# Kernel optimization log

Measured on AMD Instinct MI355X. Metric: run time of the kernel, lower is better.

Reference implementation:

```python
import jax, jax.numpy as jnp
import numpy as np

EMBED_DIM_LIST = (192, 384, 576, 768)
MAX_EMBED_DIM = 768
VOCAB = 50257
BATCH, SEQ = 8, 2048


def setup_inputs() -> dict:
    key = jax.random.key(0)
    k1, k2, k3 = jax.random.split(key, 3)
    x = jax.random.randint(k1, (BATCH, SEQ), 0, VOCAB, dtype=jnp.int64)
    weights = jax.random.uniform(k2, (len(EMBED_DIM_LIST),), dtype=jnp.float32)
    emb_weight = jax.random.normal(k3, (VOCAB, MAX_EMBED_DIM), dtype=jnp.float32) * 0.02
    return {"x": x, "weights": weights, "emb_weight": emb_weight}


def reference(x, weights, emb_weight):
    # Faithful to the non-argmax branch:
    #   mixture = sum_i pad(weights[i] * W[:, :d_i], to max_embed_dim)
    # Equivalent vectorized form: column j gets scale sum_i weights[i]*[j < d_i].
    dims = jnp.asarray(EMBED_DIM_LIST)                      # [n_choices]
    col = jnp.arange(MAX_EMBED_DIM)                          # [D]
    mask = (col[None, :] < dims[:, None]).astype(weights.dtype)  # [n_choices, D]
    col_scale = weights @ mask                               # [D]
    embedding_mixture = emb_weight * col_scale[None, :]      # [V, D]
    out = embedding_mixture[x]                               # [B, S, D] gather
    return out
```

## Files before the change

### kernel.cpp

```cpp
#include <hip/hip_runtime.h>

typedef float float4v __attribute__((ext_vector_type(4)));

__global__ void mixed_embed_kernel(const int* __restrict__ x,
                                   const float* __restrict__ w,
                                   const float* __restrict__ emb,
                                   float* __restrict__ out,
                                   int n_vec) {
    const int gid = blockIdx.x * blockDim.x + threadIdx.x;
    if (gid >= n_vec) return;

    const float w0 = w[0], w1 = w[1], w2 = w[2], w3 = w[3];

    const int token = gid / 192;
    const int d4    = gid - token * 192;
    const int row   = x[token];

    const float4v v = reinterpret_cast<const float4v*>(emb)[(long)row * 192 + d4];

    float s = w3;
    s += (d4 < 144) ? w2 : 0.0f;
    s += (d4 <  96) ? w1 : 0.0f;
    s += (d4 <  48) ? w0 : 0.0f;

    float4v o = v;
    o[0] *= s; o[1] *= s; o[2] *= s; o[3] *= s;
    __builtin_nontemporal_store(o, reinterpret_cast<float4v*>(out) + gid);
}

extern "C" void kernel_launch(void* const* d_in, const int* in_sizes, int n_in,
                              void* d_out, int out_size, void* d_ws, size_t ws_size,
                              hipStream_t stream) {
    const int*   x   = (const int*)d_in[0];
    const float* w   = (const float*)d_in[1];
    const float* emb = (const float*)d_in[2];
    float*       out = (float*)d_out;

    const int n_vec = out_size / 4;
    const int block = 256;
    const int grid  = (n_vec + block - 1) / block;

    mixed_embed_kernel<<<grid, block, 0, stream>>>(x, w, emb, out, n_vec);
}
```

Measured before the change: 21.04 us.

## Assign one wavefront per token with three float4 loads per lane

```diff
diff --git a/kernel.cpp b/kernel.cpp
--- a/kernel.cpp
+++ b/kernel.cpp
@@ -2,30 +2,40 @@
 
 typedef float float4v __attribute__((ext_vector_type(4)));
 
-__global__ void mixed_embed_kernel(const int* __restrict__ x,
-                                   const float* __restrict__ w,
-                                   const float* __restrict__ emb,
-                                   float* __restrict__ out,
-                                   int n_vec) {
-    const int gid = blockIdx.x * blockDim.x + threadIdx.x;
-    if (gid >= n_vec) return;
+__global__ void __launch_bounds__(256) mixed_embed_kernel(
+    const int* __restrict__ x,
+    const float* __restrict__ w,
+    const float* __restrict__ emb,
+    float* __restrict__ out) {
+    const int lane = threadIdx.x & 63;
+    const int wave = threadIdx.x >> 6;
+
+    int token = blockIdx.x * 4 + wave;
+    token = __builtin_amdgcn_readfirstlane(token);
+    const int row = x[token];
 
     const float w0 = w[0], w1 = w[1], w2 = w[2], w3 = w[3];
 
-    const int token = gid / 192;
-    const int d4    = gid - token * 192;
-    const int row   = x[token];
+    const float4v* __restrict__ src =
+        reinterpret_cast<const float4v*>(emb) + (long)row * 192;
+    float4v* __restrict__ dst =
+        reinterpret_cast<float4v*>(out) + (long)token * 192;
 
-    const float4v v = reinterpret_cast<const float4v*>(emb)[(long)row * 192 + d4];
+    float4v v0 = src[lane];
+    float4v v1 = src[lane + 64];
+    float4v v2 = src[lane + 128];
 
-    float s = w3;
-    s += (d4 < 144) ? w2 : 0.0f;
-    s += (d4 <  96) ? w1 : 0.0f;
-    s += (d4 <  48) ? w0 : 0.0f;
+    const float s0 = w3 + w2 + w1 + ((lane < 48) ? w0 : 0.0f);
+    const float s1 = w3 + w2 +      ((lane < 32) ? w1 : 0.0f);
+    const float s2 = w3 +           ((lane < 16) ? w2 : 0.0f);
 
-    float4v o = v;
-    o[0] *= s; o[1] *= s; o[2] *= s; o[3] *= s;
-    __builtin_nontemporal_store(o, reinterpret_cast<float4v*>(out) + gid);
+    float4v o0 = v0; o0[0] *= s0; o0[1] *= s0; o0[2] *= s0; o0[3] *= s0;
+    float4v o1 = v1; o1[0] *= s1; o1[1] *= s1; o1[2] *= s1; o1[3] *= s1;
+    float4v o2 = v2; o2[0] *= s2; o2[1] *= s2; o2[2] *= s2; o2[3] *= s2;
+
+    __builtin_nontemporal_store(o0, dst + lane);
+    __builtin_nontemporal_store(o1, dst + lane + 64);
+    __builtin_nontemporal_store(o2, dst + lane + 128);
 }
 
 extern "C" void kernel_launch(void* const* d_in, const int* in_sizes, int n_in,
@@ -36,9 +46,8 @@
     const float* emb = (const float*)d_in[2];
     float*       out = (float*)d_out;
 
-    const int n_vec = out_size / 4;
-    const int block = 256;
-    const int grid  = (n_vec + block - 1) / block;
+    const int n_tokens = out_size / 768;
+    const int grid = n_tokens / 4;
 
-    mixed_embed_kernel<<<grid, block, 0, stream>>>(x, w, emb, out, n_vec);
+    mixed_embed_kernel<<<grid, 256, 0, stream>>>(x, w, emb, out);
 }
```

Result: faster. 20.31 us (-3.4%).
